# Optimization experiments

Hardware: AMD Instinct MI355X
Metric: run time of the kernel (lower is better)

The kernel has to match this reference:

```python
import jax, jax.numpy as jnp
import numpy as np

WS = 16  # window_size

def _conv1x1(x, w, b):
    # x: [n,c,h,w], w: [out,in], b: [out]
    return jnp.einsum('nchw,oc->nohw', x, w) + b[None, :, None, None]

def _se_attention(x, w1, b1, w2, b2):
    # global avg pool -> conv -> relu -> conv -> sigmoid; returns [n,C,1,1]
    p = x.mean(axis=(2, 3), keepdims=True)
    h = jax.nn.relu(_conv1x1(p, w1, b1))
    return jax.nn.sigmoid(_conv1x1(h, w2, b2))

def setup_inputs() -> dict:
    key = jax.random.key(0)
    ks = jax.random.split(key, 13)
    B, C, H, W = 8, 96, 256, 256
    Cr = C // 3
    s = 0.02
    return {
        'x': jax.random.normal(ks[0], (B, C, H, W), jnp.float32),
        'w_real': jax.random.normal(ks[1], (C, C), jnp.float32) * s,
        'b_real': jnp.zeros((C,), jnp.float32),
        'w_imag': jax.random.normal(ks[2], (C, C), jnp.float32) * s,
        'b_imag': jnp.zeros((C,), jnp.float32),
        'car_w1': jax.random.normal(ks[3], (Cr, C), jnp.float32) * s,
        'car_b1': jnp.zeros((Cr,), jnp.float32),
        'car_w2': jax.random.normal(ks[4], (C, Cr), jnp.float32) * s,
        'car_b2': jnp.zeros((C,), jnp.float32),
        'cai_w1': jax.random.normal(ks[5], (Cr, C), jnp.float32) * s,
        'cai_b1': jnp.zeros((Cr,), jnp.float32),
        'cai_w2': jax.random.normal(ks[6], (C, Cr), jnp.float32) * s,
        'cai_b2': jnp.zeros((C,), jnp.float32),
    }

def reference(x, w_real, b_real, w_imag, b_imag,
              car_w1, car_b1, car_w2, car_b2,
              cai_w1, cai_b1, cai_w2, cai_b2):
    B, C, H, W = x.shape
    nH, nW = H // WS, W // WS
    # window partition: [B,C,H,W] -> [B*nH*nW, C, WS, WS]
    xw = x.reshape(B, C, nH, WS, nW, WS)
    xw = xw.transpose(0, 2, 4, 1, 3, 5).reshape(-1, C, WS, WS)
    # 2D FFT per window, ortho norm
    x_fft = jnp.fft.fft2(xw, norm='ortho')
    real_conv = _conv1x1(jnp.real(x_fft), w_real, b_real)
    imag_conv = _conv1x1(jnp.imag(x_fft), w_imag, b_imag)
    real_att = _se_attention(real_conv, car_w1, car_b1, car_w2, car_b2)
    imag_att = _se_attention(imag_conv, cai_w1, cai_b1, cai_w2, cai_b2)
    real_conv = real_conv * (1.0 + real_att)
    imag_conv = imag_conv * (1.0 + imag_att)
    x_fft_enh = jax.lax.complex(real_conv, imag_conv)
    x_ifft = jnp.real(jnp.fft.ifft2(x_fft_enh, norm='ortho'))
    # window merge: [B*nH*nW, C, WS, WS] -> [B,C,H,W]
    out = x_ifft.reshape(B, nH, nW, C, WS, WS)
    out = out.transpose(0, 3, 1, 4, 2, 5).reshape(B, C, H, W)
    return out
```

## Files before the change

kernel.cpp:

```cpp
#include <hip/hip_runtime.h>
#include <hip/hip_bf16.h>
#include <math.h>

#define NWIN 2048

typedef __bf16 v8bf __attribute__((ext_vector_type(8)));
typedef __bf16 v2bf __attribute__((ext_vector_type(2)));
typedef float  v4f  __attribute__((ext_vector_type(4)));
typedef unsigned int v4u __attribute__((ext_vector_type(4)));

__global__ __launch_bounds__(128) void se_alpha_kernel(
    const float* __restrict__ x,
    const float* __restrict__ w_real, const float* __restrict__ b_real,
    const float* __restrict__ car_w1, const float* __restrict__ car_b1,
    const float* __restrict__ car_w2, const float* __restrict__ car_b2,
    const float* __restrict__ b_imag,
    const float* __restrict__ cai_w1, const float* __restrict__ cai_b1,
    const float* __restrict__ cai_w2, const float* __restrict__ cai_b2,
    float* __restrict__ alpha, float* __restrict__ beta)
{
    __shared__ float wr_s[96 * 97];
    __shared__ float w1_s[32 * 97];
    __shared__ float w2_s[96 * 33];
    __shared__ float x0_s[96 * 17];
    __shared__ float pr_s[16 * 97];
    __shared__ float h1_s[16 * 33];
    const int t = threadIdx.x;
    const int blkid = blockIdx.x;

    if (blkid < 128) {
        const int b = blkid >> 4, wh = blkid & 15;
        for (int idx = t; idx < 96 * 96; idx += 128) {
            int o = idx / 96, c = idx - o * 96;
            wr_s[o * 97 + c] = w_real[idx];
        }
        for (int idx = t; idx < 32 * 96; idx += 128) {
            int j = idx / 96, c = idx - j * 96;
            w1_s[j * 97 + c] = car_w1[idx];
        }
        for (int idx = t; idx < 96 * 32; idx += 128) {
            int o = idx >> 5, j = idx & 31;
            w2_s[o * 33 + j] = car_w2[idx];
        }
        for (int idx = t; idx < 96 * 16; idx += 128) {
            int c = idx >> 4, w = idx & 15;
            x0_s[c * 17 + w] = x[(((size_t)(b * 96 + c)) * 256 + wh * 16) * 256 + w * 16];
        }
        __syncthreads();
        #pragma unroll
        for (int i = 0; i < 12; ++i) {
            int p = t + i * 128;
            int o = p >> 4, w = p & 15;
            float acc = 0.f;
            #pragma unroll 4
            for (int c = 0; c < 96; ++c) acc += wr_s[o * 97 + c] * x0_s[c * 17 + w];
            pr_s[w * 97 + o] = acc * (1.0f / 16.0f) + b_real[o];
        }
        __syncthreads();
        #pragma unroll
        for (int i = 0; i < 4; ++i) {
            int p = t + i * 128;
            int j = p >> 4, w = p & 15;
            float acc = car_b1[j];
            #pragma unroll 4
            for (int o = 0; o < 96; ++o) acc += w1_s[j * 97 + o] * pr_s[w * 97 + o];
            h1_s[w * 33 + j] = fmaxf(acc, 0.f);
        }
        __syncthreads();
        #pragma unroll
        for (int i = 0; i < 12; ++i) {
            int p = t + i * 128;
            int o = p >> 4, w = p & 15;
            float acc = car_b2[o];
            #pragma unroll
            for (int j = 0; j < 32; ++j) acc += w2_s[o * 33 + j] * h1_s[w * 33 + j];
            int n = (blkid << 4) | w;
            alpha[(size_t)n * 96 + o] = 1.f + 1.f / (1.f + __expf(-acc));
        }
    } else {
        if (t < 32) {
            float acc = cai_b1[t];
            for (int o = 0; o < 96; ++o) acc += cai_w1[t * 96 + o] * b_imag[o];
            h1_s[t] = fmaxf(acc, 0.f);
        }
        __syncthreads();
        if (t < 96) {
            float acc = cai_b2[t];
            for (int j = 0; j < 32; ++j) acc += cai_w2[t * 32 + j] * h1_s[j];
            beta[t] = 1.f + 1.f / (1.f + __expf(-acc));
        }
    }
}

__global__ __launch_bounds__(1024, 4) void wfca_main_kernel(
    const float* __restrict__ x,
    const float* __restrict__ w_real, const float* __restrict__ w_imag,
    const float* __restrict__ b_real,
    const float* __restrict__ alpha, const float* __restrict__ beta,
    float* __restrict__ out)
{
    __shared__ __bf16 wr_s[96 * 104];
    __shared__ __bf16 wi_s[96 * 104];
    __shared__ __bf16 x_lds[2][256 * 104];

    const int t    = threadIdx.x;
    const int blk  = blockIdx.x;
    const int b    = blk >> 5;
    const int wh   = (blk >> 1) & 15;
    const int ww0  = (blk & 1) * 8;

    const int lane = t & 63;
    const int l16  = lane & 15;
    const int quad = lane >> 4;
    const int wv   = t >> 6;
    const int hf   = (16 - wv) & 15;
    const int wf   = (16 - l16) & 15;

    const int sw = t & 15;
    const int g  = t >> 4;

    const float* xb = x + (((size_t)(b * 96)) << 16) + (size_t)(wh * 16) * 256;

    float st0[12], st1[12];

    auto stage_issue = [&](int win_) {
        const float* xp = xb + (ww0 + win_) * 16 + sw;
        #pragma unroll
        for (int i = 0; i < 12; ++i) {
            int j = g * 12 + i;
            int cp = j >> 4, h = j & 15;
            const float* p = xp + (((size_t)(2 * cp)) << 16) + h * 256;
            st0[i] = p[0];
            st1[i] = p[65536];
        }
    };
    auto stage_write = [&](int bufsel) {
        #pragma unroll
        for (int i = 0; i < 12; ++i) {
            int j = g * 12 + i;
            int cp = j >> 4, h = j & 15;
            v2bf pk;
            pk[0] = (__bf16)st0[i];
            pk[1] = (__bf16)st1[i];
            *(v2bf*)&x_lds[bufsel][(h * 16 + sw) * 104 + 2 * cp] = pk;
        }
    };

    stage_issue(0);
    {
        float wrv[9], wiv[9], btv[9];
        #pragma unroll
        for (int r = 0; r < 9; ++r) {
            int idx = t + r * 1024;
            wrv[r] = w_real[idx];
            wiv[r] = w_imag[idx];
            btv[r] = beta[idx / 96];
        }
        #pragma unroll
        for (int r = 0; r < 9; ++r) {
            int idx = t + r * 1024;
            int o = idx / 96, c = idx - o * 96;
            wr_s[o * 104 + c] = (__bf16)(0.5f * wrv[r]);
            wi_s[o * 104 + c] = (__bf16)(0.5f * btv[r] * wiv[r]);
        }
    }
    stage_write(0);
    __syncthreads();

    int cur = 0;
    for (int win = 0; win < 8; ++win) {
        float af[6];
        #pragma unroll
        for (int n = 0; n < 6; ++n)
            af[n] = alpha[(size_t)(blk * 8 + win) * 96 + n * 16 + l16];

        if (win < 7) stage_issue(win + 1);

        v4f acc[6];
        #pragma unroll
        for (int n = 0; n < 6; ++n) acc[n] = v4f{0.f, 0.f, 0.f, 0.f};

        const __bf16* xl = x_lds[cur];
        #pragma unroll
        for (int k = 0; k < 3; ++k) {
            const int c0 = k * 32;
            v8bf a_x = *(const v8bf*)&xl[(wv * 16 + l16) * 104 + c0 + quad * 8];
            v8bf a_f = *(const v8bf*)&xl[(hf * 16 + wf) * 104 + c0 + quad * 8];
            v4u fu = __builtin_bit_cast(v4u, a_f);
            const v4u sm = {0x80008000u, 0x80008000u, 0x80008000u, 0x80008000u};
            v8bf a_fn = __builtin_bit_cast(v8bf, fu ^ sm);

            #pragma unroll
            for (int n = 0; n < 6; ++n) {
                v8bf bwr = *(const v8bf*)&wr_s[(n * 16 + l16) * 104 + c0 + quad * 8];
                v8bf bwi = *(const v8bf*)&wi_s[(n * 16 + l16) * 104 + c0 + quad * 8];
                acc[n] = __builtin_amdgcn_mfma_f32_16x16x32_bf16(a_x,  bwi, acc[n], 0, 0, 0);
                acc[n] = __builtin_amdgcn_mfma_f32_16x16x32_bf16(a_fn, bwi, acc[n], 0, 0, 0);
                v4f utmp = __builtin_amdgcn_mfma_f32_16x16x32_bf16(
                               a_x, bwr, v4f{0.f, 0.f, 0.f, 0.f}, 0, 0, 0);
                utmp = __builtin_amdgcn_mfma_f32_16x16x32_bf16(a_f, bwr, utmp, 0, 0, 0);
                #pragma unroll
                for (int r = 0; r < 4; ++r) acc[n][r] += af[n] * utmp[r];
            }
        }

        {
            const int col = (ww0 + win) * 16;
            #pragma unroll
            for (int n = 0; n < 6; ++n) {
                const int o = n * 16 + l16;
                v4f v = acc[n];
                if (wv == 0 && quad == 0) {
                    v[0] += 16.f * af[n] * b_real[o];
                }
                size_t idx = (((size_t)(b * 96 + o)) * 256 + wh * 16 + wv) * 256
                             + col + quad * 4;
                *(v4f*)(out + idx) = v;
            }
        }

        if (win < 7) {
            stage_write(cur ^ 1);
            __syncthreads();
            cur ^= 1;
        }
    }
}

extern "C" void kernel_launch(void* const* d_in, const int* in_sizes, int n_in,
                              void* d_out, int out_size, void* d_ws, size_t ws_size,
                              hipStream_t stream) {
    const float* x      = (const float*)d_in[0];
    const float* w_real = (const float*)d_in[1];
    const float* b_real = (const float*)d_in[2];
    const float* w_imag = (const float*)d_in[3];
    const float* b_imag = (const float*)d_in[4];
    const float* car_w1 = (const float*)d_in[5];
    const float* car_b1 = (const float*)d_in[6];
    const float* car_w2 = (const float*)d_in[7];
    const float* car_b2 = (const float*)d_in[8];
    const float* cai_w1 = (const float*)d_in[9];
    const float* cai_b1 = (const float*)d_in[10];
    const float* cai_w2 = (const float*)d_in[11];
    const float* cai_b2 = (const float*)d_in[12];
    float* out = (float*)d_out;

    float* alpha = (float*)d_ws;
    float* beta  = alpha + NWIN * 96;

    se_alpha_kernel<<<129, 128, 0, stream>>>(
        x, w_real, b_real, car_w1, car_b1, car_w2, car_b2,
        b_imag, cai_w1, cai_b1, cai_w2, cai_b2, alpha, beta);

    wfca_main_kernel<<<256, 1024, 0, stream>>>(
        x, w_real, w_imag, b_real, alpha, beta, out);
}
```

Before: 505.5 us.

## Stream x tiles into LDS via async global_load_lds with per-chunk triple buffering

After: 466.9 us. 1.08x faster.

```diff
diff --git a/kernel.cpp b/kernel.cpp
--- a/kernel.cpp
+++ b/kernel.cpp
@@ -7,7 +7,6 @@
 typedef __bf16 v8bf __attribute__((ext_vector_type(8)));
 typedef __bf16 v2bf __attribute__((ext_vector_type(2)));
 typedef float  v4f  __attribute__((ext_vector_type(4)));
-typedef unsigned int v4u __attribute__((ext_vector_type(4)));
 
 __global__ __launch_bounds__(128) void se_alpha_kernel(
     const float* __restrict__ x,
@@ -101,7 +100,8 @@
 {
     __shared__ __bf16 wr_s[96 * 104];
     __shared__ __bf16 wi_s[96 * 104];
-    __shared__ __bf16 x_lds[2][256 * 104];
+    __shared__ float  xf[3][32 * 256];
+    __shared__ float  alpha_s[768];
 
     const int t    = threadIdx.x;
     const int blk  = blockIdx.x;
@@ -116,37 +116,22 @@
     const int hf   = (16 - wv) & 15;
     const int wf   = (16 - l16) & 15;
 
-    const int sw = t & 15;
-    const int g  = t >> 4;
-
-    const float* xb = x + (((size_t)(b * 96)) << 16) + (size_t)(wh * 16) * 256;
-
-    float st0[12], st1[12];
-
-    auto stage_issue = [&](int win_) {
-        const float* xp = xb + (ww0 + win_) * 16 + sw;
-        #pragma unroll
-        for (int i = 0; i < 12; ++i) {
-            int j = g * 12 + i;
-            int cp = j >> 4, h = j & 15;
-            const float* p = xp + (((size_t)(2 * cp)) << 16) + h * 256;
-            st0[i] = p[0];
-            st1[i] = p[65536];
+    auto issue = [&](int w_, int k_) {
+        #pragma unroll
+        for (int u = 0; u < 2; ++u) {
+            const int cl  = 2 * wv + u;
+            const int swz = (cl >> 3) & 3;
+            const float* g = x
+                + (((size_t)(b * 96 + k_ * 32 + cl)) << 16)
+                + (size_t)(wh * 16 + ((lane >> 2) ^ swz)) * 256
+                + (ww0 + w_) * 16 + 4 * (lane & 3);
+            float* l = &xf[k_][cl * 256];
+            __builtin_amdgcn_global_load_lds(
+                (const __attribute__((address_space(1))) float*)g,
+                (__attribute__((address_space(3))) float*)l, 16, 0, 0);
         }
     };
-    auto stage_write = [&](int bufsel) {
-        #pragma unroll
-        for (int i = 0; i < 12; ++i) {
-            int j = g * 12 + i;
-            int cp = j >> 4, h = j & 15;
-            v2bf pk;
-            pk[0] = (__bf16)st0[i];
-            pk[1] = (__bf16)st1[i];
-            *(v2bf*)&x_lds[bufsel][(h * 16 + sw) * 104 + 2 * cp] = pk;
-        }
-    };
-
-    stage_issue(0);
+
     {
         float wrv[9], wiv[9], btv[9];
         #pragma unroll
@@ -164,32 +149,53 @@
             wi_s[o * 104 + c] = (__bf16)(0.5f * btv[r] * wiv[r]);
         }
     }
-    stage_write(0);
+    if (t < 768) alpha_s[t] = alpha[(size_t)blk * 768 + t];
+    float brv[6];
+    #pragma unroll
+    for (int n = 0; n < 6; ++n) brv[n] = b_real[n * 16 + l16];
     __syncthreads();
 
-    int cur = 0;
+    issue(0, 0);
+    issue(0, 1);
+
+    const int pxq = (wv * 16 + l16) ^ (quad << 4);
+    const int pfq = (hf * 16 + wf) ^ (quad << 4);
+
     for (int win = 0; win < 8; ++win) {
         float af[6];
-        #pragma unroll
-        for (int n = 0; n < 6; ++n)
-            af[n] = alpha[(size_t)(blk * 8 + win) * 96 + n * 16 + l16];
-
-        if (win < 7) stage_issue(win + 1);
-
         v4f acc[6];
         #pragma unroll
-        for (int n = 0; n < 6; ++n) acc[n] = v4f{0.f, 0.f, 0.f, 0.f};
-
-        const __bf16* xl = x_lds[cur];
+        for (int n = 0; n < 6; ++n) {
+            af[n]  = alpha_s[win * 96 + n * 16 + l16];
+            acc[n] = v4f{0.f, 0.f, 0.f, 0.f};
+        }
         #pragma unroll
         for (int k = 0; k < 3; ++k) {
+            if (win == 7 && k == 2)      asm volatile("s_waitcnt vmcnt(0)" ::: "memory");
+            else if (win == 0 || k == 2) asm volatile("s_waitcnt vmcnt(2)" ::: "memory");
+            else                         asm volatile("s_waitcnt vmcnt(8)" ::: "memory");
+            __builtin_amdgcn_s_barrier();
+            __builtin_amdgcn_sched_barrier(0);
+
+            if (k == 0)      issue(win, 2);
+            else if (k == 1) { if (win < 7) issue(win + 1, 0); }
+            else             { if (win < 7) issue(win + 1, 1); }
+
+            const float* xk = xf[k];
+            float fx[8], ff[8];
+            #pragma unroll
+            for (int j = 0; j < 8; ++j) {
+                fx[j] = xk[(quad * 8 + j) * 256 + pxq];
+                ff[j] = xk[(quad * 8 + j) * 256 + pfq];
+            }
+            v8bf a_x, a_f, a_fn;
+            #pragma unroll
+            for (int j = 0; j < 8; ++j) {
+                a_x[j]  = (__bf16)fx[j];
+                a_f[j]  = (__bf16)ff[j];
+                a_fn[j] = (__bf16)(-ff[j]);
+            }
             const int c0 = k * 32;
-            v8bf a_x = *(const v8bf*)&xl[(wv * 16 + l16) * 104 + c0 + quad * 8];
-            v8bf a_f = *(const v8bf*)&xl[(hf * 16 + wf) * 104 + c0 + quad * 8];
-            v4u fu = __builtin_bit_cast(v4u, a_f);
-            const v4u sm = {0x80008000u, 0x80008000u, 0x80008000u, 0x80008000u};
-            v8bf a_fn = __builtin_bit_cast(v8bf, fu ^ sm);
-
             #pragma unroll
             for (int n = 0; n < 6; ++n) {
                 v8bf bwr = *(const v8bf*)&wr_s[(n * 16 + l16) * 104 + c0 + quad * 8];
@@ -211,18 +217,12 @@
                 const int o = n * 16 + l16;
                 v4f v = acc[n];
                 if (wv == 0 && quad == 0) {
-                    v[0] += 16.f * af[n] * b_real[o];
+                    v[0] += 16.f * af[n] * brv[n];
                 }
                 size_t idx = (((size_t)(b * 96 + o)) * 256 + wh * 16 + wv) * 256
                              + col + quad * 4;
                 *(v4f*)(out + idx) = v;
             }
-        }
-
-        if (win < 7) {
-            stage_write(cur ^ 1);
-            __syncthreads();
-            cur ^= 1;
         }
     }
 }
```
